# Optimization experiments

Measured on AMD Instinct MI355X. Metric: run time of the kernel, lower is better.

## Reference

```python
import jax, jax.numpy as jnp
import numpy as np

B, C, H, W = 16, 64, 256, 256
RED = 16


def setup_inputs() -> dict:
    key = jax.random.key(0)
    ks = jax.random.split(key, 7)
    x = jax.random.normal(ks[0], (B, C, H, W), dtype=jnp.float32)
    # rowwise grouped conv: Conv2d(C, C, kernel=(1,C), groups=C) -> per-channel weight row [C, C] + bias [C]
    Wrow = jax.random.normal(ks[1], (C, C), dtype=jnp.float32) * 0.02
    brow = jax.random.normal(ks[2], (C,), dtype=jnp.float32) * 0.02
    # conv_du: 1x1 convs acting on [B,C,1,1] == dense layers
    W1 = jax.random.normal(ks[3], (RED, C), dtype=jnp.float32) * 0.05
    b1 = jnp.zeros((RED,), dtype=jnp.float32)
    W2 = jax.random.normal(ks[4], (C, RED), dtype=jnp.float32) * 0.05
    b2 = jnp.zeros((C,), dtype=jnp.float32)
    return {"x": x, "Wrow": Wrow, "brow": brow, "W1": W1, "b1": b1, "W2": W2, "b2": b2}


def reference(x, Wrow, brow, W1, b1, W2, b2):
    b, c, h, w = x.shape
    n = h * w
    # ChannelFO: global average pool -> [B, C]
    pool = jnp.mean(x, axis=(2, 3))
    # ChannelSO: channel covariance corr[b,i,j] = sum_hw x[b,i]*x[b,j] / n
    xf = x.reshape(b, c, n)
    corr = jnp.einsum('bcn,bdn->bcd', xf, xf) / n  # [B, C, C]
    # grouped (1,C) conv over [B,C,1,C]: per-channel dot of corr row with its weight row
    so = jnp.einsum('bcd,cd->bc', corr, Wrow) + brow  # [B, C]
    y = pool + so  # [B, C]  (== [B,C,1,1] squeezed)
    # conv_du: 1x1 conv -> ReLU -> 1x1 conv -> Sigmoid
    z = jax.nn.relu(y @ W1.T + b1)          # [B, RED]
    g = jax.nn.sigmoid(z @ W2.T + b2)       # [B, C]
    return x * g[:, :, None, None]
```

## Files before the change

kernel.cpp:

```cpp
#include <hip/hip_runtime.h>
#include <math.h>

#define Bn   16
#define Cn   64
#define Nn   65536
#define Sn   64
#define Ln   (Nn / Sn)
#define REDn 16

typedef float    f32x4  __attribute__((ext_vector_type(4)));
typedef float    f32x16 __attribute__((ext_vector_type(16)));
typedef __fp16   fp16x2 __attribute__((ext_vector_type(2)));
typedef _Float16 f16x8  __attribute__((ext_vector_type(8)));

union half8_u {
  f16x8  v;
  fp16x2 h[4];
};

__global__ __launch_bounds__(256, 4) void gram_pool_kernel(
    const float* __restrict__ x, const float* __restrict__ Wrow,
    float* __restrict__ part) {
  const int b    = blockIdx.x / Sn;
  const int s    = blockIdx.x % Sn;
  const int tid  = threadIdx.x;
  const int wid  = tid >> 6;
  const int lane = tid & 63;
  const int l31  = lane & 31;
  const int lhi  = lane >> 5;
  const int rr   = lane >> 2;
  const int cc   = lane & 3;

  const float* xb = x + (size_t)b * Cn * Nn;

  __shared__ float stage[4][Cn * 17];
  __shared__ float corr_s[Cn][Cn + 1];
  __shared__ float pool_lds0[4][32];
  __shared__ float pool_lds1[4][32];

  float* wb = &stage[wid][0];

  const float* gsrc[4];
  int widx[4];
#pragma unroll
  for (int i = 0; i < 4; ++i) {
    const int row = 16 * i + rr;
    gsrc[i] = xb + (size_t)row * Nn + cc * 4;
    widx[i] = row * 17 + cc * 4;
  }
  const int fA = l31 * 17 + lhi * 8;
  const int fB = (l31 + 32) * 17 + lhi * 8;

  const int kw = s * Ln + wid * (Ln / 4);

  f32x16 acc00, acc01, acc11;
#pragma unroll
  for (int r = 0; r < 16; ++r) { acc00[r] = 0.f; acc01[r] = 0.f; acc11[r] = 0.f; }
  float pool0 = 0.f, pool1 = 0.f;
  const fp16x2 one2 = {(__fp16)1.0f, (__fp16)1.0f};

  f32x4 sA[4], sB[4], sC[4];
#pragma unroll
  for (int i = 0; i < 4; ++i) sA[i] = *(const f32x4*)(gsrc[i] + kw);
#pragma unroll
  for (int i = 0; i < 4; ++i) sB[i] = *(const f32x4*)(gsrc[i] + kw + 16);
#pragma unroll
  for (int i = 0; i < 4; ++i) sC[i] = *(const f32x4*)(gsrc[i] + kw + 32);

  auto step = [&](f32x4* stg, int t) {
#pragma unroll
    for (int i = 0; i < 4; ++i) *(f32x4*)&wb[widx[i]] = stg[i];
    if (t < 13) {
      const int ko = kw + (t + 3) * 16;
#pragma unroll
      for (int i = 0; i < 4; ++i) stg[i] = *(const f32x4*)(gsrc[i] + ko);
    }
    f32x4 a0 = *(const f32x4*)&wb[fA];
    f32x4 a1 = *(const f32x4*)&wb[fA + 4];
    f32x4 c0 = *(const f32x4*)&wb[fB];
    f32x4 c1 = *(const f32x4*)&wb[fB + 4];

    half8_u au, bu;
    au.h[0] = __builtin_amdgcn_cvt_pkrtz(a0[0], a0[1]);
    au.h[1] = __builtin_amdgcn_cvt_pkrtz(a0[2], a0[3]);
    au.h[2] = __builtin_amdgcn_cvt_pkrtz(a1[0], a1[1]);
    au.h[3] = __builtin_amdgcn_cvt_pkrtz(a1[2], a1[3]);
    bu.h[0] = __builtin_amdgcn_cvt_pkrtz(c0[0], c0[1]);
    bu.h[1] = __builtin_amdgcn_cvt_pkrtz(c0[2], c0[3]);
    bu.h[2] = __builtin_amdgcn_cvt_pkrtz(c1[0], c1[1]);
    bu.h[3] = __builtin_amdgcn_cvt_pkrtz(c1[2], c1[3]);

#pragma unroll
    for (int i = 0; i < 4; ++i) {
      pool0 = __builtin_amdgcn_fdot2(au.h[i], one2, pool0, false);
      pool1 = __builtin_amdgcn_fdot2(bu.h[i], one2, pool1, false);
    }

    acc00 = __builtin_amdgcn_mfma_f32_32x32x16_f16(au.v, au.v, acc00, 0, 0, 0);
    acc01 = __builtin_amdgcn_mfma_f32_32x32x16_f16(au.v, bu.v, acc01, 0, 0, 0);
    acc11 = __builtin_amdgcn_mfma_f32_32x32x16_f16(bu.v, bu.v, acc11, 0, 0, 0);
  };

#pragma unroll
  for (int tp = 0; tp < 5; ++tp) {
    step(sA, 3 * tp);
    step(sB, 3 * tp + 1);
    step(sC, 3 * tp + 2);
  }
  step(sA, 15);

  pool0 += __shfl_down(pool0, 32);
  pool1 += __shfl_down(pool1, 32);
  if (lane < 32) {
    pool_lds0[wid][lane] = pool0;
    pool_lds1[wid][lane] = pool1;
  }

  for (int w = 0; w < 4; ++w) {
    __syncthreads();
    if (wid == w) {
#pragma unroll
      for (int r = 0; r < 16; ++r) {
        const int i = (r & 3) + 8 * (r >> 2) + 4 * lhi;
        const int j = l31;
        if (w == 0) {
          corr_s[i][j]           = acc00[r];
          corr_s[i][j + 32]      = acc01[r];
          corr_s[j + 32][i]      = acc01[r];
          corr_s[i + 32][j + 32] = acc11[r];
        } else {
          corr_s[i][j]           += acc00[r];
          corr_s[i][j + 32]      += acc01[r];
          corr_s[j + 32][i]      += acc01[r];
          corr_s[i + 32][j + 32] += acc11[r];
        }
      }
    }
  }
  __syncthreads();

  if (tid < Cn) {
    const float* wr = Wrow + tid * Cn;
    float so = 0.f;
#pragma unroll 8
    for (int d = 0; d < Cn; ++d) so += corr_s[tid][d] * wr[d];
    float pp = 0.f;
    if (tid < 32) {
#pragma unroll
      for (int w = 0; w < 4; ++w) pp += pool_lds0[w][tid];
    } else {
#pragma unroll
      for (int w = 0; w < 4; ++w) pp += pool_lds1[w][tid - 32];
    }
    float* o = part + (size_t)(b * Sn + s) * (2 * Cn);
    o[tid]      = so;
    o[Cn + tid] = pp;
  }
}

__global__ __launch_bounds__(64) void se_kernel(
    const float* __restrict__ part, const float* __restrict__ brow,
    const float* __restrict__ W1, const float* __restrict__ b1,
    const float* __restrict__ W2, const float* __restrict__ b2,
    float* __restrict__ g) {
  const int b = blockIdx.x;
  const int t = threadIdx.x;

  __shared__ float y_s[Cn];
  __shared__ float z_s[REDn];

  float so = 0.f, pl = 0.f;
  for (int s = 0; s < Sn; ++s) {
    const float* p = part + (size_t)(b * Sn + s) * (2 * Cn);
    so += p[t];
    pl += p[Cn + t];
  }
  y_s[t] = (so + pl) * (1.0f / (float)Nn) + brow[t];
  __syncthreads();

  if (t < REDn) {
    float z = b1[t];
#pragma unroll 8
    for (int c = 0; c < Cn; ++c) z += W1[t * Cn + c] * y_s[c];
    z_s[t] = fmaxf(z, 0.f);
  }
  __syncthreads();

  float a = b2[t];
#pragma unroll
  for (int r = 0; r < REDn; ++r) a += W2[t * REDn + r] * z_s[r];
  g[b * Cn + t] = 1.0f / (1.0f + expf(-a));
}

#define SGRID 4096
__global__ __launch_bounds__(256) void scale_kernel(
    const float* __restrict__ x, const float* __restrict__ g,
    float* __restrict__ out) {
  const int    bid   = blockIdx.x;
  const size_t base4 = (size_t)bid * 4096;
  const float  gg    = g[bid >> 2];

  const f32x4* xv = (const f32x4*)x + base4;
  f32x4*       ov = (f32x4*)out + base4;
  const int t = threadIdx.x;

  f32x4 v0 = xv[t];
  f32x4 v1 = xv[t + 256];
  f32x4 v2 = xv[t + 512];
  f32x4 v3 = xv[t + 768];
#pragma unroll
  for (int it = 0; it < 4; ++it) {
    const int cur = t + it * 1024;
    f32x4 w0 = v0, w1 = v1, w2 = v2, w3 = v3;
    if (it < 3) {
      const int nxt = cur + 1024;
      v0 = xv[nxt];
      v1 = xv[nxt + 256];
      v2 = xv[nxt + 512];
      v3 = xv[nxt + 768];
    }
    w0 *= gg; w1 *= gg; w2 *= gg; w3 *= gg;
    __builtin_nontemporal_store(w0, &ov[cur]);
    __builtin_nontemporal_store(w1, &ov[cur + 256]);
    __builtin_nontemporal_store(w2, &ov[cur + 512]);
    __builtin_nontemporal_store(w3, &ov[cur + 768]);
  }
}

extern "C" void kernel_launch(void* const* d_in, const int* in_sizes, int n_in,
                              void* d_out, int out_size, void* d_ws, size_t ws_size,
                              hipStream_t stream) {
  const float* x    = (const float*)d_in[0];
  const float* Wrow = (const float*)d_in[1];
  const float* brow = (const float*)d_in[2];
  const float* W1   = (const float*)d_in[3];
  const float* b1   = (const float*)d_in[4];
  const float* W2   = (const float*)d_in[5];
  const float* b2   = (const float*)d_in[6];
  float* out = (float*)d_out;

  float* part = (float*)d_out;
  float* g    = (float*)d_ws;

  gram_pool_kernel<<<Bn * Sn, 256, 0, stream>>>(x, Wrow, part);
  se_kernel<<<Bn, 64, 0, stream>>>(part, brow, W1, b1, W2, b2, g);
  scale_kernel<<<SGRID, 256, 0, stream>>>(x, g, out);
}
```

Measured before the change: 153.9 us.

## Share double-buffered LDS tile across warps with block-wide barrier pipeline

```diff
diff --git a/kernel.cpp b/kernel.cpp
--- a/kernel.cpp
+++ b/kernel.cpp
@@ -6,6 +6,9 @@
 #define Nn   65536
 #define Sn   64
 #define Ln   (Nn / Sn)
+#define KT   64
+#define NT   (Ln / KT)
+#define LW   68
 #define REDn 16
 
 typedef float    f32x4  __attribute__((ext_vector_type(4)));
@@ -28,30 +31,26 @@
   const int lane = tid & 63;
   const int l31  = lane & 31;
   const int lhi  = lane >> 5;
-  const int rr   = lane >> 2;
-  const int cc   = lane & 3;
 
   const float* xb = x + (size_t)b * Cn * Nn;
 
-  __shared__ float stage[4][Cn * 17];
-  __shared__ float corr_s[Cn][Cn + 1];
+  __shared__ float buf[2][Cn * LW];
   __shared__ float pool_lds0[4][32];
   __shared__ float pool_lds1[4][32];
 
-  float* wb = &stage[wid][0];
-
   const float* gsrc[4];
-  int widx[4];
+  int wof[4];
 #pragma unroll
   for (int i = 0; i < 4; ++i) {
-    const int row = 16 * i + rr;
-    gsrc[i] = xb + (size_t)row * Nn + cc * 4;
-    widx[i] = row * 17 + cc * 4;
-  }
-  const int fA = l31 * 17 + lhi * 8;
-  const int fB = (l31 + 32) * 17 + lhi * 8;
-
-  const int kw = s * Ln + wid * (Ln / 4);
+    const int row = i * 16 + (tid >> 4);
+    const int g   = tid & 15;
+    gsrc[i] = xb + (size_t)row * Nn + g * 4;
+    wof[i]  = row * LW + g * 4;
+  }
+  const int fA = l31 * LW + wid * 16 + lhi * 8;
+  const int fB = (l31 + 32) * LW + wid * 16 + lhi * 8;
+
+  const int k0 = s * Ln;
 
   f32x16 acc00, acc01, acc11;
 #pragma unroll
@@ -59,55 +58,60 @@
   float pool0 = 0.f, pool1 = 0.f;
   const fp16x2 one2 = {(__fp16)1.0f, (__fp16)1.0f};
 
-  f32x4 sA[4], sB[4], sC[4];
-#pragma unroll
-  for (int i = 0; i < 4; ++i) sA[i] = *(const f32x4*)(gsrc[i] + kw);
-#pragma unroll
-  for (int i = 0; i < 4; ++i) sB[i] = *(const f32x4*)(gsrc[i] + kw + 16);
-#pragma unroll
-  for (int i = 0; i < 4; ++i) sC[i] = *(const f32x4*)(gsrc[i] + kw + 32);
-
-  auto step = [&](f32x4* stg, int t) {
-#pragma unroll
-    for (int i = 0; i < 4; ++i) *(f32x4*)&wb[widx[i]] = stg[i];
-    if (t < 13) {
-      const int ko = kw + (t + 3) * 16;
-#pragma unroll
-      for (int i = 0; i < 4; ++i) stg[i] = *(const f32x4*)(gsrc[i] + ko);
-    }
-    f32x4 a0 = *(const f32x4*)&wb[fA];
-    f32x4 a1 = *(const f32x4*)&wb[fA + 4];
-    f32x4 c0 = *(const f32x4*)&wb[fB];
-    f32x4 c1 = *(const f32x4*)&wb[fB + 4];
-
-    half8_u au, bu;
-    au.h[0] = __builtin_amdgcn_cvt_pkrtz(a0[0], a0[1]);
-    au.h[1] = __builtin_amdgcn_cvt_pkrtz(a0[2], a0[3]);
-    au.h[2] = __builtin_amdgcn_cvt_pkrtz(a1[0], a1[1]);
-    au.h[3] = __builtin_amdgcn_cvt_pkrtz(a1[2], a1[3]);
-    bu.h[0] = __builtin_amdgcn_cvt_pkrtz(c0[0], c0[1]);
-    bu.h[1] = __builtin_amdgcn_cvt_pkrtz(c0[2], c0[3]);
-    bu.h[2] = __builtin_amdgcn_cvt_pkrtz(c1[0], c1[1]);
-    bu.h[3] = __builtin_amdgcn_cvt_pkrtz(c1[2], c1[3]);
-
-#pragma unroll
-    for (int i = 0; i < 4; ++i) {
-      pool0 = __builtin_amdgcn_fdot2(au.h[i], one2, pool0, false);
-      pool1 = __builtin_amdgcn_fdot2(bu.h[i], one2, pool1, false);
-    }
-
-    acc00 = __builtin_amdgcn_mfma_f32_32x32x16_f16(au.v, au.v, acc00, 0, 0, 0);
-    acc01 = __builtin_amdgcn_mfma_f32_32x32x16_f16(au.v, bu.v, acc01, 0, 0, 0);
-    acc11 = __builtin_amdgcn_mfma_f32_32x32x16_f16(bu.v, bu.v, acc11, 0, 0, 0);
-  };
-
-#pragma unroll
-  for (int tp = 0; tp < 5; ++tp) {
-    step(sA, 3 * tp);
-    step(sB, 3 * tp + 1);
-    step(sC, 3 * tp + 2);
-  }
-  step(sA, 15);
+  f32x4 st[3][4];
+#pragma unroll
+  for (int q = 0; q < 3; ++q)
+#pragma unroll
+    for (int i = 0; i < 4; ++i)
+      st[q][i] = *(const f32x4*)(gsrc[i] + k0 + q * KT);
+#pragma unroll
+  for (int i = 0; i < 4; ++i) *(f32x4*)&buf[0][wof[i]] = st[0][i];
+  asm volatile("s_waitcnt lgkmcnt(0)" ::: "memory");
+  __builtin_amdgcn_s_barrier();
+
+#pragma unroll
+  for (int t = 0; t < NT; ++t) {
+    const int p = t & 1;
+    if (t + 3 < NT) {
+#pragma unroll
+      for (int i = 0; i < 4; ++i)
+        st[t % 3][i] = *(const f32x4*)(gsrc[i] + k0 + (t + 3) * KT);
+    }
+    if (t + 1 < NT) {
+#pragma unroll
+      for (int i = 0; i < 4; ++i)
+        *(f32x4*)&buf[p ^ 1][wof[i]] = st[(t + 1) % 3][i];
+    }
+    {
+      const float* wb = &buf[p][0];
+      f32x4 a0 = *(const f32x4*)(wb + fA);
+      f32x4 a1 = *(const f32x4*)(wb + fA + 4);
+      f32x4 c0 = *(const f32x4*)(wb + fB);
+      f32x4 c1 = *(const f32x4*)(wb + fB + 4);
+
+      half8_u au, bu;
+      au.h[0] = __builtin_amdgcn_cvt_pkrtz(a0[0], a0[1]);
+      au.h[1] = __builtin_amdgcn_cvt_pkrtz(a0[2], a0[3]);
+      au.h[2] = __builtin_amdgcn_cvt_pkrtz(a1[0], a1[1]);
+      au.h[3] = __builtin_amdgcn_cvt_pkrtz(a1[2], a1[3]);
+      bu.h[0] = __builtin_amdgcn_cvt_pkrtz(c0[0], c0[1]);
+      bu.h[1] = __builtin_amdgcn_cvt_pkrtz(c0[2], c0[3]);
+      bu.h[2] = __builtin_amdgcn_cvt_pkrtz(c1[0], c1[1]);
+      bu.h[3] = __builtin_amdgcn_cvt_pkrtz(c1[2], c1[3]);
+
+#pragma unroll
+      for (int i = 0; i < 4; ++i) {
+        pool0 = __builtin_amdgcn_fdot2(au.h[i], one2, pool0, false);
+        pool1 = __builtin_amdgcn_fdot2(bu.h[i], one2, pool1, false);
+      }
+
+      acc00 = __builtin_amdgcn_mfma_f32_32x32x16_f16(au.v, au.v, acc00, 0, 0, 0);
+      acc01 = __builtin_amdgcn_mfma_f32_32x32x16_f16(au.v, bu.v, acc01, 0, 0, 0);
+      acc11 = __builtin_amdgcn_mfma_f32_32x32x16_f16(bu.v, bu.v, acc11, 0, 0, 0);
+    }
+    asm volatile("s_waitcnt lgkmcnt(0)" ::: "memory");
+    __builtin_amdgcn_s_barrier();
+  }
 
   pool0 += __shfl_down(pool0, 32);
   pool1 += __shfl_down(pool1, 32);
@@ -116,6 +120,7 @@
     pool_lds1[wid][lane] = pool1;
   }
 
+  float (*corr)[Cn + 1] = (float(*)[Cn + 1])&buf[0][0];
   for (int w = 0; w < 4; ++w) {
     __syncthreads();
     if (wid == w) {
@@ -124,15 +129,15 @@
         const int i = (r & 3) + 8 * (r >> 2) + 4 * lhi;
         const int j = l31;
         if (w == 0) {
-          corr_s[i][j]           = acc00[r];
-          corr_s[i][j + 32]      = acc01[r];
-          corr_s[j + 32][i]      = acc01[r];
-          corr_s[i + 32][j + 32] = acc11[r];
+          corr[i][j]           = acc00[r];
+          corr[i][j + 32]      = acc01[r];
+          corr[j + 32][i]      = acc01[r];
+          corr[i + 32][j + 32] = acc11[r];
         } else {
-          corr_s[i][j]           += acc00[r];
-          corr_s[i][j + 32]      += acc01[r];
-          corr_s[j + 32][i]      += acc01[r];
-          corr_s[i + 32][j + 32] += acc11[r];
+          corr[i][j]           += acc00[r];
+          corr[i][j + 32]      += acc01[r];
+          corr[j + 32][i]      += acc01[r];
+          corr[i + 32][j + 32] += acc11[r];
         }
       }
     }
@@ -143,7 +148,7 @@
     const float* wr = Wrow + tid * Cn;
     float so = 0.f;
 #pragma unroll 8
-    for (int d = 0; d < Cn; ++d) so += corr_s[tid][d] * wr[d];
+    for (int d = 0; d < Cn; ++d) so += corr[tid][d] * wr[d];
     float pp = 0.f;
     if (tid < 32) {
 #pragma unroll
```

After: 133.9 us. 13.0% less time.
